# Optimization experiments

Measured on AMD Instinct MI355X. Metric: run time of the kernel, lower is better.

Reference implementation:

```python
import jax, jax.numpy as jnp
import numpy as np
from jax import lax

B, L, D = 2, 1024, 1024
EXPAND, N, K = 2, 16, 4          # expand, d_state, d_conv
DI = EXPAND * D                  # d_inner = 2048
R = (D + 15) // 16               # dt_rank = 64
EPS = 1e-5


def setup_inputs() -> dict:
    key = jax.random.key(0)
    ks = jax.random.split(key, 8)
    x = jax.random.normal(ks[0], (B, L, D), dtype=jnp.float32)
    ln_w = jnp.ones((D,), jnp.float32)
    ln_b = jnp.zeros((D,), jnp.float32)
    W_in = jax.random.normal(ks[1], (D, 2 * DI), jnp.float32) * (1.0 / np.sqrt(D))
    conv_w = jax.random.normal(ks[2], (DI, K), jnp.float32) * 0.2
    conv_b = jnp.zeros((DI,), jnp.float32)
    W_x = jax.random.normal(ks[3], (DI, R + 2 * N), jnp.float32) * (1.0 / np.sqrt(DI))
    W_dt = jax.random.normal(ks[4], (R, DI), jnp.float32) * (1.0 / np.sqrt(R))
    b_dt = jnp.full((DI,), -4.0, jnp.float32)  # softplus(-4) ~ 0.018 dt init
    A_log = jnp.log(jnp.broadcast_to(jnp.arange(1, N + 1, dtype=jnp.float32), (DI, N)))
    D_param = jnp.ones((DI,), jnp.float32)
    W_out = jax.random.normal(ks[5], (DI, D), jnp.float32) * (1.0 / np.sqrt(DI))
    return {"x": x, "ln_w": ln_w, "ln_b": ln_b, "W_in": W_in, "conv_w": conv_w,
            "conv_b": conv_b, "W_x": W_x, "W_dt": W_dt, "b_dt": b_dt,
            "A_log": A_log, "D_param": D_param, "W_out": W_out}


def _mamba_block(x, ln_w, ln_b, W_in, conv_w, conv_b, W_x, W_dt, b_dt, A_log, D_param, W_out):
    # pre-LayerNorm
    mu = jnp.mean(x, axis=-1, keepdims=True)
    xc = x - mu
    var = jnp.mean(xc * xc, axis=-1, keepdims=True)
    h = xc * lax.rsqrt(var + EPS) * ln_w + ln_b          # [B,L,D]

    xz = h @ W_in                                        # [B,L,2*DI]
    xi, z = xz[..., :DI], xz[..., DI:]

    # depthwise causal conv1d, kernel K, left pad K-1
    xp = jnp.pad(xi, ((0, 0), (K - 1, 0), (0, 0)))
    conv = conv_b
    for k in range(K):
        conv = conv + xp[:, k:k + L, :] * conv_w[:, k]
    u = jax.nn.silu(conv)                                # [B,L,DI]

    proj = u @ W_x                                       # [B,L,R+2N]
    dt_r = proj[..., :R]
    Bm = proj[..., R:R + N]                              # [B,L,N]
    Cm = proj[..., R + N:]                               # [B,L,N]
    dt = jax.nn.softplus(dt_r @ W_dt + b_dt)             # [B,L,DI]

    A = -jnp.exp(A_log)                                  # [DI,N]
    dA = jnp.exp(dt[..., None] * A)                      # [B,L,DI,N]
    dBu = (dt * u)[..., None] * Bm[:, :, None, :]        # [B,L,DI,N]

    def comb(e1, e2):
        a1, b1 = e1
        a2, b2 = e2
        return a1 * a2, a2 * b1 + b2

    _, hs = lax.associative_scan(comb, (dA, dBu), axis=1)  # [B,L,DI,N]
    y = jnp.einsum('bldn,bln->bld', hs, Cm) + u * D_param
    y = y * jax.nn.silu(z)
    return x + y @ W_out


def reference(x, ln_w, ln_b, W_in, conv_w, conv_b, W_x, W_dt, b_dt, A_log, D_param, W_out):
    return _mamba_block(x, ln_w, ln_b, W_in, conv_w, conv_b, W_x, W_dt, b_dt,
                        A_log, D_param, W_out)
```

## Files before the change

kernel.cpp:

```cpp
#include <hip/hip_runtime.h>
#include <hip/hip_bf16.h>
#include <math.h>

#define B_ 2
#define L_ 1024
#define D_ 1024
#define DI_ 2048
#define K_ 4
#define N_ 16
#define R_ 64
#define BL_ (B_ * L_)
#define EPS_ 1e-5f

#define IDX4(l) ((l) + (((l) >> 6) << 2))

typedef __attribute__((ext_vector_type(8))) short short8;
typedef __attribute__((ext_vector_type(4))) float f32x4;

__device__ inline unsigned short f2bf(float f) {
    unsigned u = __float_as_uint(f);
    unsigned r = (u + 0x7fffu + ((u >> 16) & 1u)) >> 16;
    return (unsigned short)r;
}
__device__ inline float bf2f(unsigned short s) {
    return __uint_as_float(((unsigned)s) << 16);
}
__device__ inline float fast_silu(float z) {
    return z * __builtin_amdgcn_rcpf(1.f + __expf(-z));
}
__device__ inline void gl_lds16(const void* g, void* l) {
    __builtin_amdgcn_global_load_lds(
        (const __attribute__((address_space(1))) void*)g,
        (__attribute__((address_space(3))) void*)l, 16, 0, 0);
}

template <int CTRL>
__device__ inline float dpp_shr(float x) {
    return __int_as_float(__builtin_amdgcn_update_dpp(
        0, __float_as_int(x), CTRL, 0xf, 0xf, true));
}
__device__ inline float row16_sum(float p) {
    p += dpp_shr<0x111>(p);
    p += dpp_shr<0x112>(p);
    p += dpp_shr<0x114>(p);
    p += dpp_shr<0x118>(p);
    return p;
}

__global__ void ln_kernel(const float* __restrict__ x, const float* __restrict__ w,
                          const float* __restrict__ b, unsigned short* __restrict__ hb) {
    int row = blockIdx.x;
    const float* xr = x + (size_t)row * D_;
    float4 v = ((const float4*)xr)[threadIdx.x];

    __shared__ float red[4];
    float s = v.x + v.y + v.z + v.w;
    for (int off = 1; off < 64; off <<= 1) s += __shfl_xor(s, off, 64);
    if ((threadIdx.x & 63) == 0) red[threadIdx.x >> 6] = s;
    __syncthreads();
    float mu = (red[0] + red[1] + red[2] + red[3]) * (1.0f / D_);
    __syncthreads();
    float cx = v.x - mu, cy = v.y - mu, cz = v.z - mu, cw = v.w - mu;
    float sq = cx*cx + cy*cy + cz*cz + cw*cw;
    for (int off = 1; off < 64; off <<= 1) sq += __shfl_xor(sq, off, 64);
    if ((threadIdx.x & 63) == 0) red[threadIdx.x >> 6] = sq;
    __syncthreads();
    float var = (red[0] + red[1] + red[2] + red[3]) * (1.0f / D_);
    float rstd = rsqrtf(var + EPS_);

    float4 wv = ((const float4*)w)[threadIdx.x];
    float4 bv = ((const float4*)b)[threadIdx.x];
    ushort4 o;
    o.x = f2bf(cx * rstd * wv.x + bv.x);
    o.y = f2bf(cy * rstd * wv.y + bv.y);
    o.z = f2bf(cz * rstd * wv.z + bv.z);
    o.w = f2bf(cw * rstd * wv.w + bv.w);
    ((ushort4*)(hb + (size_t)row * D_))[threadIdx.x] = o;
}

__global__ void transpose_cast_all(const float* __restrict__ W_in, const float* __restrict__ W_x,
                                   const float* __restrict__ W_out,
                                   unsigned short* __restrict__ WinT, unsigned short* __restrict__ WxT,
                                   unsigned short* __restrict__ WoutT) {
    int bid = blockIdx.x;
    const float* W; unsigned short* WT; int K, N, bx, by;
    if (bid < 4096)      { W = W_in;  WT = WinT;  K = 1024; N = 4096; bx = bid & 127; by = bid >> 7; }
    else if (bid < 4288) { int id = bid - 4096; W = W_x;  WT = WxT;  K = DI_; N = 96;   bx = id % 3;  by = id / 3; }
    else                 { int id = bid - 4288; W = W_out; WT = WoutT; K = DI_; N = 1024; bx = id & 31; by = id >> 5; }
    __shared__ float tile[32][33];
    int k0 = by * 32, n0 = bx * 32;
    int tr = threadIdx.x >> 5;
    int tc = threadIdx.x & 31;
#pragma unroll
    for (int i = 0; i < 4; ++i)
        tile[tr + i*8][tc] = W[(size_t)(k0 + tr + i*8) * N + n0 + tc];
    __syncthreads();
#pragma unroll
    for (int i = 0; i < 4; ++i)
        WT[(size_t)(n0 + tr + i*8) * K + k0 + tc] = f2bf(tile[tc][tr + i*8]);
}

template <int BN, int MODE>
__global__ __launch_bounds__(256) void mfma_gemm_bt(
        const unsigned short* __restrict__ A,  int lda,
        const unsigned short* __restrict__ BT, int ldb,
        float* __restrict__ C, int ldc, int Kchunk,
        float* __restrict__ xi, unsigned short* __restrict__ sz) {
    constexpr int NT = BN / 32;
    __shared__ unsigned short As[128 * 32];
    __shared__ unsigned short Bs[BN * 32];

    int tid = threadIdx.x;
    int wave = tid >> 6, lane = tid & 63;
    int lane15 = lane & 15, quad = lane >> 4;
    int wr = wave >> 1, wc = wave & 1;

    int m0 = blockIdx.y * 128;
    int n0 = blockIdx.x * BN;
    int kbeg = blockIdx.z * Kchunk;
    int kend = kbeg + Kchunk;

    f32x4 acc[4][NT];
#pragma unroll
    for (int i = 0; i < 4; ++i)
#pragma unroll
        for (int j = 0; j < NT; ++j) acc[i][j] = (f32x4){0.f, 0.f, 0.f, 0.f};

    constexpr int ACALLS = 8;
    constexpr int BCALLS = BN * 4 / 64;

    for (int k0 = kbeg; k0 < kend; k0 += 32) {
        __syncthreads();
        for (int c = wave; c < ACALLS + BCALLS; c += 4) {
            if (c < ACALLS) {
                int cell = c * 64 + lane;
                int m = cell >> 2, s = cell & 3;
                int q = s ^ (m & 3) ^ ((m >> 2) & 3);
                gl_lds16(A + (size_t)(m0 + m) * lda + k0 + q * 8, &As[c * 512]);
            } else {
                int cell = (c - ACALLS) * 64 + lane;
                int n = cell >> 2, s = cell & 3;
                int q = s ^ (n & 3) ^ ((n >> 2) & 3);
                gl_lds16(BT + (size_t)(n0 + n) * ldb + k0 + q * 8, &Bs[(c - ACALLS) * 512]);
            }
        }
        __syncthreads();

        short8 af[4], bfr[NT];
#pragma unroll
        for (int i = 0; i < 4; ++i) {
            int m = wr * 64 + i * 16 + lane15;
            int s = quad ^ (m & 3) ^ ((m >> 2) & 3);
            af[i] = *(const short8*)&As[m * 32 + s * 8];
        }
#pragma unroll
        for (int j = 0; j < NT; ++j) {
            int n = wc * (NT * 16) + j * 16 + lane15;
            int s = quad ^ (n & 3) ^ ((n >> 2) & 3);
            bfr[j] = *(const short8*)&Bs[n * 32 + s * 8];
        }
#pragma unroll
        for (int i = 0; i < 4; ++i)
#pragma unroll
            for (int j = 0; j < NT; ++j)
                acc[i][j] = __builtin_amdgcn_mfma_f32_16x16x32_bf16(af[i], bfr[j], acc[i][j], 0, 0, 0);
    }

#pragma unroll
    for (int i = 0; i < 4; ++i) {
        int row = m0 + wr * 64 + i * 16 + quad * 4;
#pragma unroll
        for (int j = 0; j < NT; ++j) {
            int col = n0 + wc * (NT * 16) + j * 16 + lane15;
#pragma unroll
            for (int r = 0; r < 4; ++r) {
                float v = acc[i][j][r];
                int rr = row + r;
                if (MODE == 0) {
                    C[(size_t)rr * ldc + col] = v;
                } else if (MODE == 1) {
                    atomicAdd(&C[(size_t)rr * ldc + col], v);
                } else {
                    if (col < DI_) xi[(size_t)rr * DI_ + col] = v;
                    else           sz[(size_t)rr * DI_ + (col - DI_)] = f2bf(fast_silu(v));
                }
            }
        }
    }
}

__global__ void conv_silu_kernel(const float* __restrict__ xi, const float* __restrict__ cw,
                                 const float* __restrict__ cb, unsigned short* __restrict__ ub) {
    int idx = blockIdx.x * blockDim.x + threadIdx.x;
    int c = idx & (DI_ - 1);
    int bl = idx >> 11;
    int l = bl & (L_ - 1);
    float4 w4 = ((const float4*)cw)[c];
    float acc = cb[c];
    const float* base = xi + (size_t)bl * DI_ + c;
    if (l >= 3) {
        acc = fmaf(base[-(size_t)3 * DI_], w4.x, acc);
        acc = fmaf(base[-(size_t)2 * DI_], w4.y, acc);
        acc = fmaf(base[-(size_t)1 * DI_], w4.z, acc);
        acc = fmaf(base[0],                w4.w, acc);
    } else {
        if (l >= 2) acc = fmaf(*(base - 2 * DI_), w4.y, acc);
        if (l >= 1) acc = fmaf(*(base - 1 * DI_), w4.z, acc);
        acc = fmaf(base[0], w4.w, acc);
    }
    ub[idx] = f2bf(fast_silu(acc));
}

__global__ __launch_bounds__(256) void dtprep(
        const float* __restrict__ proj, const float* __restrict__ W_dt,
        const float* __restrict__ b_dt, const unsigned short* __restrict__ ub,
        const unsigned short* __restrict__ szb, const float* __restrict__ Dp,
        float2* __restrict__ dtduT, unsigned int* __restrict__ szdT) {
    __shared__ alignas(16) unsigned char smem[64 * 65 * 8];
    float (*As)[68] = reinterpret_cast<float(*)[68]>(smem);
    float (*Bs)[64] = reinterpret_cast<float(*)[64]>(smem + 4352);
    float2 (*T2)[65] = reinterpret_cast<float2(*)[65]>(smem);
    unsigned int (*TU)[65] = reinterpret_cast<unsigned int(*)[65]>(smem);

    int tid = threadIdx.x;
    int n0 = blockIdx.x * 64;
    int m0 = blockIdx.y * 64;
    int ar = tid >> 2, ak = (tid & 3) << 2;
    int kb = tid >> 4, bc = (tid & 15) << 2;
    int ty = tid >> 4, tx = tid & 15;

    float acc[4][4] = {};
#pragma unroll
    for (int k0 = 0; k0 < R_; k0 += 16) {
        float4 av = *(const float4*)&proj[(size_t)(m0 + ar) * 96 + k0 + ak];
        As[ak + 0][ar] = av.x; As[ak + 1][ar] = av.y;
        As[ak + 2][ar] = av.z; As[ak + 3][ar] = av.w;
        float4 bv = *(const float4*)&W_dt[(size_t)(k0 + kb) * DI_ + n0 + bc];
        Bs[kb][bc + 0] = bv.x; Bs[kb][bc + 1] = bv.y;
        Bs[kb][bc + 2] = bv.z; Bs[kb][bc + 3] = bv.w;
        __syncthreads();
#pragma unroll
        for (int kk = 0; kk < 16; ++kk) {
            float a[4], bb[4];
#pragma unroll
            for (int i = 0; i < 4; ++i) a[i] = As[kk][ty * 4 + i];
#pragma unroll
            for (int j = 0; j < 4; ++j) bb[j] = Bs[kk][tx * 4 + j];
#pragma unroll
            for (int i = 0; i < 4; ++i)
#pragma unroll
                for (int j = 0; j < 4; ++j)
                    acc[i][j] = fmaf(a[i], bb[j], acc[i][j]);
        }
        __syncthreads();
    }

    float4 bd = *(const float4*)&b_dt[n0 + tx * 4];
    float4 dp4 = *(const float4*)&Dp[n0 + tx * 4];
    float bda[4] = {bd.x, bd.y, bd.z, bd.w};
    float dpa[4] = {dp4.x, dp4.y, dp4.z, dp4.w};
    float2 d2[4][4];
    unsigned int su[4][4];
#pragma unroll
    for (int i = 0; i < 4; ++i) {
        int bl = m0 + ty * 4 + i;
        ushort4 u4 = *(const ushort4*)&ub[(size_t)bl * DI_ + n0 + tx * 4];
        ushort4 s4 = *(const ushort4*)&szb[(size_t)bl * DI_ + n0 + tx * 4];
        unsigned short ua[4] = {u4.x, u4.y, u4.z, u4.w};
        unsigned short sa[4] = {s4.x, s4.y, s4.z, s4.w};
#pragma unroll
        for (int j = 0; j < 4; ++j) {
            float v = acc[i][j] + bda[j];
            float dtv = fmaxf(v, 0.f) + __logf(1.f + __expf(-fabsf(v)));
            float uu = bf2f(ua[j]);
            float szv = bf2f(sa[j]);
            d2[i][j] = make_float2(dtv, dtv * uu);
            su[i][j] = ((unsigned)f2bf(uu * dpa[j] * szv) << 16) | (unsigned)f2bf(szv);
        }
    }

#pragma unroll
    for (int i = 0; i < 4; ++i)
#pragma unroll
        for (int j = 0; j < 4; ++j)
            T2[ty * 4 + i][tx * 4 + j] = d2[i][j];
    __syncthreads();
#pragma unroll
    for (int i = 0; i < 8; ++i) {
        int c_l = (tid >> 5) + i * 8;
#pragma unroll
        for (int jj = 0; jj < 2; ++jj) {
            int bl_l = (tid & 31) + jj * 32;
            dtduT[(size_t)(n0 + c_l) * BL_ + m0 + bl_l] = T2[bl_l][c_l];
        }
    }
    __syncthreads();

#pragma unroll
    for (int i = 0; i < 4; ++i)
#pragma unroll
        for (int j = 0; j < 4; ++j)
            TU[ty * 4 + i][tx * 4 + j] = su[i][j];
    __syncthreads();
#pragma unroll
    for (int i = 0; i < 8; ++i) {
        int c_l = (tid >> 5) + i * 8;
#pragma unroll
        for (int jj = 0; jj < 2; ++jj) {
            int bl_l = (tid & 31) + jj * 32;
            szdT[(size_t)(n0 + c_l) * BL_ + m0 + bl_l] = TU[bl_l][c_l];
        }
    }
}

__global__ __launch_bounds__(256) void scan_v5(
        const float2* __restrict__ dtduT, const unsigned int* __restrict__ szdT,
        const float* __restrict__ proj, const float* __restrict__ A_log,
        unsigned short* __restrict__ yzT) {
    int bc = blockIdx.x;
    int b = bc >> 10;
    int cp = bc & 1023;
    int t = threadIdx.x;
    int n = t & 15;
    int cs = (t >> 4) & 1;
    int chunk = t >> 5;
    int c = cp * 2 + cs;

    __shared__ float dd[2][(L_ + 32) * 2];
    __shared__ float sA[8][32];
    __shared__ float sB[8][32];
    __shared__ float ps[2][L_ + 64];

    {
        int half = t >> 7;
        int tt = t & 127;
        int l = tt * 8;
        int cload = cp * 2 + half;
        const float4* g = (const float4*)(dtduT + (size_t)cload * BL_ + (size_t)b * L_ + l);
        int il2 = l + ((l >> 6) << 1);
        float* dst = &dd[half][il2 * 2];
        *(float4*)(dst + 0)  = g[0];
        *(float4*)(dst + 4)  = g[1];
        *(float4*)(dst + 8)  = g[2];
        *(float4*)(dst + 12) = g[3];
    }
    __syncthreads();

    float A = -__expf(A_log[c * N_ + n]);
    int l0 = chunk * 128;
    const float* pB = proj + (size_t)b * L_ * 96 + R_ + n;
    const float* pC = pB + N_;

    float a = 1.f, acc = 0.f;
#pragma unroll
    for (int h = 0; h < 2; ++h) {
        int lb = l0 + h * 64;
        const float* ddp = &dd[cs][(lb + ((lb >> 6) << 1)) * 2];
        const float* pBb = pB + (size_t)lb * 96;
#pragma unroll
        for (int q = 0; q < 16; ++q) {
            float4 d0 = *(const float4*)(ddp + q * 8);
            float4 d1 = *(const float4*)(ddp + q * 8 + 4);
            float b0 = pBb[(q*4 + 0) * 96];
            float b1 = pBb[(q*4 + 1) * 96];
            float b2 = pBb[(q*4 + 2) * 96];
            float b3 = pBb[(q*4 + 3) * 96];
            float e;
            e = __expf(d0.x * A); a *= e; acc = fmaf(e, acc, d0.y * b0);
            e = __expf(d0.z * A); a *= e; acc = fmaf(e, acc, d0.w * b1);
            e = __expf(d1.x * A); a *= e; acc = fmaf(e, acc, d1.y * b2);
            e = __expf(d1.z * A); a *= e; acc = fmaf(e, acc, d1.w * b3);
        }
    }
    sA[chunk][t & 31] = a;
    sB[chunk][t & 31] = acc;
    __syncthreads();

    if (t < 32) {
        float hc = 0.f;
#pragma unroll
        for (int j = 0; j < 8; ++j) {
            float aj = sA[j][t];
            float bj = sB[j][t];
            sB[j][t] = hc;
            hc = fmaf(aj, hc, bj);
        }
    }
    __syncthreads();
    float h = sB[chunk][t & 31];

#pragma unroll
    for (int hh = 0; hh < 2; ++hh) {
        int lb = l0 + hh * 64;
        const float* ddp = &dd[cs][(lb + ((lb >> 6) << 1)) * 2];
        const float* pBb = pB + (size_t)lb * 96;
        const float* pCb = pC + (size_t)lb * 96;
        float* psb = &ps[cs][IDX4(lb)];
#pragma unroll
        for (int q = 0; q < 16; ++q) {
            float4 d0 = *(const float4*)(ddp + q * 8);
            float4 d1 = *(const float4*)(ddp + q * 8 + 4);
            float b0 = pBb[(q*4 + 0) * 96], c0 = pCb[(q*4 + 0) * 96];
            float b1 = pBb[(q*4 + 1) * 96], c1 = pCb[(q*4 + 1) * 96];
            float b2 = pBb[(q*4 + 2) * 96], c2 = pCb[(q*4 + 2) * 96];
            float b3 = pBb[(q*4 + 3) * 96], c3 = pCb[(q*4 + 3) * 96];
            float e, p0, p1, p2, p3;
            e = __expf(d0.x * A); h = fmaf(e, h, d0.y * b0); p0 = row16_sum(h * c0);
            e = __expf(d0.z * A); h = fmaf(e, h, d0.w * b1); p1 = row16_sum(h * c1);
            e = __expf(d1.x * A); h = fmaf(e, h, d1.y * b2); p2 = row16_sum(h * c2);
            e = __expf(d1.z * A); h = fmaf(e, h, d1.w * b3); p3 = row16_sum(h * c3);
            if (n == 15) *(float4*)&psb[q * 4] = (float4){p0, p1, p2, p3};
        }
    }
    __syncthreads();

    {
        int half = t >> 7;
        int tt = t & 127;
        int l = tt * 8;
        int c_out = cp * 2 + half;
        size_t tb = (size_t)c_out * BL_ + (size_t)b * L_;
        const float* pp = &ps[half][IDX4(l)];
        ushort4 o[2];
#pragma unroll
        for (int g = 0; g < 2; ++g) {
            float4 p4 = *(const float4*)(pp + g * 4);
            uint4 sd4 = *(const uint4*)(szdT + tb + l + g * 4);
            o[g].x = f2bf(p4.x * bf2f((unsigned short)(sd4.x & 0xffff)) + bf2f((unsigned short)(sd4.x >> 16)));
            o[g].y = f2bf(p4.y * bf2f((unsigned short)(sd4.y & 0xffff)) + bf2f((unsigned short)(sd4.y >> 16)));
            o[g].z = f2bf(p4.z * bf2f((unsigned short)(sd4.z & 0xffff)) + bf2f((unsigned short)(sd4.z >> 16)));
            o[g].w = f2bf(p4.w * bf2f((unsigned short)(sd4.w & 0xffff)) + bf2f((unsigned short)(sd4.w >> 16)));
        }
        *(ushort4*)(yzT + tb + l) = o[0];
        *(ushort4*)(yzT + tb + l + 4) = o[1];
    }
}

__global__ void transpose_y(const unsigned short* __restrict__ yzT, unsigned short* __restrict__ yz) {
    __shared__ unsigned short t[32][33];
    int c0 = blockIdx.y * 32, bl0 = blockIdx.x * 32;
    int r = threadIdx.x >> 5;
    int col = threadIdx.x & 31;
#pragma unroll
    for (int i = 0; i < 4; ++i)
        t[r + i*8][col] = yzT[(size_t)(c0 + r + i*8) * BL_ + bl0 + col];
    __syncthreads();
#pragma unroll
    for (int i = 0; i < 4; ++i)
        yz[(size_t)(bl0 + r + i*8) * DI_ + c0 + col] = t[col][r + i*8];
}

extern "C" void kernel_launch(void* const* d_in, const int* in_sizes, int n_in,
                              void* d_out, int out_size, void* d_ws, size_t ws_size,
                              hipStream_t stream) {
    const float* x       = (const float*)d_in[0];
    const float* ln_w    = (const float*)d_in[1];
    const float* ln_b    = (const float*)d_in[2];
    const float* W_in    = (const float*)d_in[3];
    const float* conv_w  = (const float*)d_in[4];
    const float* conv_b  = (const float*)d_in[5];
    const float* W_x     = (const float*)d_in[6];
    const float* W_dt    = (const float*)d_in[7];
    const float* b_dt    = (const float*)d_in[8];
    const float* A_log   = (const float*)d_in[9];
    const float* D_param = (const float*)d_in[10];
    const float* W_out   = (const float*)d_in[11];
    float* out = (float*)d_out;

    uint8_t* p = (uint8_t*)d_ws;
    unsigned short* hb    = (unsigned short*)p;  p += (size_t)BL_ * D_ * 2;
    unsigned short* WinT  = (unsigned short*)p;  p += (size_t)4096 * 1024 * 2;
    float*          xib   = (float*)p;           p += (size_t)BL_ * DI_ * 4;
    unsigned short* szb   = (unsigned short*)p;  p += (size_t)BL_ * DI_ * 2;
    unsigned short* ub    = (unsigned short*)p;  p += (size_t)BL_ * DI_ * 2;
    unsigned short* WxT   = (unsigned short*)p;  p += (size_t)96 * DI_ * 2;
    float*          proj  = (float*)p;           p += (size_t)BL_ * 96 * 4;
    unsigned short* WoutT = (unsigned short*)p;  p += (size_t)1024 * DI_ * 2;
    float2*         dtduT = (float2*)p;          p += (size_t)BL_ * DI_ * 8;
    unsigned int*   szdT  = (unsigned int*)p;    p += (size_t)BL_ * DI_ * 4;
    unsigned short* yzT   = (unsigned short*)p;  p += (size_t)BL_ * DI_ * 2;
    unsigned short* yzb   = (unsigned short*)d_ws;

    hipMemsetAsync(proj, 0, (size_t)BL_ * 96 * 4, stream);
    hipMemcpyAsync(out, x, (size_t)BL_ * D_ * 4, hipMemcpyDeviceToDevice, stream);

    transpose_cast_all<<<6336, 256, 0, stream>>>(W_in, W_x, W_out, WinT, WxT, WoutT);

    ln_kernel<<<BL_, 256, 0, stream>>>(x, ln_w, ln_b, hb);

    mfma_gemm_bt<128, 3><<<dim3(4096 / 128, BL_ / 128, 1), 256, 0, stream>>>(
        hb, 1024, WinT, 1024, nullptr, 0, 1024, xib, szb);

    conv_silu_kernel<<<(BL_ * DI_) / 256, 256, 0, stream>>>(xib, conv_w, conv_b, ub);

    mfma_gemm_bt<96, 1><<<dim3(1, BL_ / 128, 16), 256, 0, stream>>>(
        ub, DI_, WxT, DI_, proj, 96, 128, nullptr, nullptr);

    dtprep<<<dim3(DI_ / 64, BL_ / 64), 256, 0, stream>>>(
        proj, W_dt, b_dt, ub, szb, D_param, dtduT, szdT);

    scan_v5<<<B_ * DI_ / 2, 256, 0, stream>>>(dtduT, szdT, proj, A_log, yzT);

    transpose_y<<<dim3(BL_ / 32, DI_ / 32), 256, 0, stream>>>(yzT, yzb);

    mfma_gemm_bt<128, 1><<<dim3(1024 / 128, BL_ / 128, 2), 256, 0, stream>>>(
        yzb, DI_, WoutT, DI_, out, 1024, 1024, nullptr, nullptr);
}
```

Before: 285.6 us.

## Transpose B/C to contiguous layout and run scan with one channel per block

A new small kernel transposes the B and C columns of proj into [b][n][l] arrays, so each scan thread reads them as contiguous float4 instead of scalar loads strided by 96. The scan now gives each block a single channel with 16 chunks of 64 steps, which doubles the block count, shortens each thread's sequential work, and adds a launch-bounds occupancy hint. The exponentials become hardware exp2 with log2(e) folded into A. In exchange there is one extra kernel launch, a longer 16-step chunk-carry pass, and BT/CT are placed in a workspace region assumed not to overlap live buffers.

```diff
diff --git a/kernel.cpp b/kernel.cpp
--- a/kernel.cpp
+++ b/kernel.cpp
@@ -28,6 +28,11 @@
 __device__ inline float fast_silu(float z) {
     return z * __builtin_amdgcn_rcpf(1.f + __expf(-z));
 }
+#if __has_builtin(__builtin_amdgcn_exp2f)
+__device__ inline float fexp2(float x) { return __builtin_amdgcn_exp2f(x); }
+#else
+__device__ inline float fexp2(float x) { return exp2f(x); }
+#endif
 __device__ inline void gl_lds16(const void* g, void* l) {
     __builtin_amdgcn_global_load_lds(
         (const __attribute__((address_space(1))) void*)g,
@@ -313,73 +318,79 @@
     }
 }
 
-__global__ __launch_bounds__(256) void scan_v5(
+__global__ void bc_transpose(const float* __restrict__ proj,
+                             float* __restrict__ BT, float* __restrict__ CT) {
+    __shared__ float t[32][33];
+    int bl0 = blockIdx.x * 32;
+    int b = bl0 >> 10;
+    int l0 = bl0 & (L_ - 1);
+    int r = threadIdx.x >> 5;
+    int col = threadIdx.x & 31;
+#pragma unroll
+    for (int i = 0; i < 4; ++i)
+        t[r + i*8][col] = proj[(size_t)(bl0 + r + i*8) * 96 + R_ + col];
+    __syncthreads();
+#pragma unroll
+    for (int i = 0; i < 4; ++i) {
+        int n = r + i*8;
+        float v = t[col][n];
+        if (n < N_) BT[((size_t)b * N_ + n) * L_ + l0 + col] = v;
+        else        CT[((size_t)b * N_ + (n - N_)) * L_ + l0 + col] = v;
+    }
+}
+
+__global__ __launch_bounds__(256, 6) void scan_v6(
         const float2* __restrict__ dtduT, const unsigned int* __restrict__ szdT,
-        const float* __restrict__ proj, const float* __restrict__ A_log,
-        unsigned short* __restrict__ yzT) {
+        const float* __restrict__ BT, const float* __restrict__ CT,
+        const float* __restrict__ A_log, unsigned short* __restrict__ yzT) {
     int bc = blockIdx.x;
-    int b = bc >> 10;
-    int cp = bc & 1023;
+    int b = bc >> 11;
+    int c = bc & (DI_ - 1);
     int t = threadIdx.x;
     int n = t & 15;
-    int cs = (t >> 4) & 1;
-    int chunk = t >> 5;
-    int c = cp * 2 + cs;
-
-    __shared__ float dd[2][(L_ + 32) * 2];
-    __shared__ float sA[8][32];
-    __shared__ float sB[8][32];
-    __shared__ float ps[2][L_ + 64];
+    int chunk = t >> 4;
+
+    __shared__ float dd[(L_ + 32) * 2];
+    __shared__ float sA[16][16];
+    __shared__ float sB[16][16];
+    __shared__ float ps[L_ + 64];
 
     {
-        int half = t >> 7;
-        int tt = t & 127;
-        int l = tt * 8;
-        int cload = cp * 2 + half;
-        const float4* g = (const float4*)(dtduT + (size_t)cload * BL_ + (size_t)b * L_ + l);
+        int l = t * 4;
+        const float4* g = (const float4*)(dtduT + (size_t)c * BL_ + (size_t)b * L_ + l);
         int il2 = l + ((l >> 6) << 1);
-        float* dst = &dd[half][il2 * 2];
-        *(float4*)(dst + 0)  = g[0];
-        *(float4*)(dst + 4)  = g[1];
-        *(float4*)(dst + 8)  = g[2];
-        *(float4*)(dst + 12) = g[3];
-    }
-    __syncthreads();
-
-    float A = -__expf(A_log[c * N_ + n]);
-    int l0 = chunk * 128;
-    const float* pB = proj + (size_t)b * L_ * 96 + R_ + n;
-    const float* pC = pB + N_;
+        float* dst = &dd[il2 * 2];
+        *(float4*)(dst + 0) = g[0];
+        *(float4*)(dst + 4) = g[1];
+    }
+    __syncthreads();
+
+    float A2 = -__expf(A_log[c * N_ + n]) * 1.4426950408889634f;
+    int lb = chunk * 64;
+    const float* ddp = &dd[(lb + ((lb >> 6) << 1)) * 2];
+    const float4* pB4 = (const float4*)(BT + ((size_t)b * N_ + n) * L_ + lb);
+    const float4* pC4 = (const float4*)(CT + ((size_t)b * N_ + n) * L_ + lb);
 
     float a = 1.f, acc = 0.f;
 #pragma unroll
-    for (int h = 0; h < 2; ++h) {
-        int lb = l0 + h * 64;
-        const float* ddp = &dd[cs][(lb + ((lb >> 6) << 1)) * 2];
-        const float* pBb = pB + (size_t)lb * 96;
-#pragma unroll
-        for (int q = 0; q < 16; ++q) {
-            float4 d0 = *(const float4*)(ddp + q * 8);
-            float4 d1 = *(const float4*)(ddp + q * 8 + 4);
-            float b0 = pBb[(q*4 + 0) * 96];
-            float b1 = pBb[(q*4 + 1) * 96];
-            float b2 = pBb[(q*4 + 2) * 96];
-            float b3 = pBb[(q*4 + 3) * 96];
-            float e;
-            e = __expf(d0.x * A); a *= e; acc = fmaf(e, acc, d0.y * b0);
-            e = __expf(d0.z * A); a *= e; acc = fmaf(e, acc, d0.w * b1);
-            e = __expf(d1.x * A); a *= e; acc = fmaf(e, acc, d1.y * b2);
-            e = __expf(d1.z * A); a *= e; acc = fmaf(e, acc, d1.w * b3);
-        }
-    }
-    sA[chunk][t & 31] = a;
-    sB[chunk][t & 31] = acc;
-    __syncthreads();
-
-    if (t < 32) {
+    for (int q = 0; q < 16; ++q) {
+        float4 d0 = *(const float4*)(ddp + q * 8);
+        float4 d1 = *(const float4*)(ddp + q * 8 + 4);
+        float4 b4 = pB4[q];
+        float e;
+        e = fexp2(d0.x * A2); a *= e; acc = fmaf(e, acc, d0.y * b4.x);
+        e = fexp2(d0.z * A2); a *= e; acc = fmaf(e, acc, d0.w * b4.y);
+        e = fexp2(d1.x * A2); a *= e; acc = fmaf(e, acc, d1.y * b4.z);
+        e = fexp2(d1.z * A2); a *= e; acc = fmaf(e, acc, d1.w * b4.w);
+    }
+    sA[chunk][n] = a;
+    sB[chunk][n] = acc;
+    __syncthreads();
+
+    if (t < 16) {
         float hc = 0.f;
 #pragma unroll
-        for (int j = 0; j < 8; ++j) {
+        for (int j = 0; j < 16; ++j) {
             float aj = sA[j][t];
             float bj = sB[j][t];
             sB[j][t] = hc;
@@ -387,52 +398,36 @@
         }
     }
     __syncthreads();
-    float h = sB[chunk][t & 31];
-
-#pragma unroll
-    for (int hh = 0; hh < 2; ++hh) {
-        int lb = l0 + hh * 64;
-        const float* ddp = &dd[cs][(lb + ((lb >> 6) << 1)) * 2];
-        const float* pBb = pB + (size_t)lb * 96;
-        const float* pCb = pC + (size_t)lb * 96;
-        float* psb = &ps[cs][IDX4(lb)];
-#pragma unroll
-        for (int q = 0; q < 16; ++q) {
-            float4 d0 = *(const float4*)(ddp + q * 8);
-            float4 d1 = *(const float4*)(ddp + q * 8 + 4);
-            float b0 = pBb[(q*4 + 0) * 96], c0 = pCb[(q*4 + 0) * 96];
-            float b1 = pBb[(q*4 + 1) * 96], c1 = pCb[(q*4 + 1) * 96];
-            float b2 = pBb[(q*4 + 2) * 96], c2 = pCb[(q*4 + 2) * 96];
-            float b3 = pBb[(q*4 + 3) * 96], c3 = pCb[(q*4 + 3) * 96];
-            float e, p0, p1, p2, p3;
-            e = __expf(d0.x * A); h = fmaf(e, h, d0.y * b0); p0 = row16_sum(h * c0);
-            e = __expf(d0.z * A); h = fmaf(e, h, d0.w * b1); p1 = row16_sum(h * c1);
-            e = __expf(d1.x * A); h = fmaf(e, h, d1.y * b2); p2 = row16_sum(h * c2);
-            e = __expf(d1.z * A); h = fmaf(e, h, d1.w * b3); p3 = row16_sum(h * c3);
-            if (n == 15) *(float4*)&psb[q * 4] = (float4){p0, p1, p2, p3};
-        }
+    float h = sB[chunk][n];
+
+    float* psb = &ps[IDX4(lb)];
+#pragma unroll
+    for (int q = 0; q < 16; ++q) {
+        float4 d0 = *(const float4*)(ddp + q * 8);
+        float4 d1 = *(const float4*)(ddp + q * 8 + 4);
+        float4 b4 = pB4[q];
+        float4 c4 = pC4[q];
+        float e, p0, p1, p2, p3;
+        e = fexp2(d0.x * A2); h = fmaf(e, h, d0.y * b4.x); p0 = row16_sum(h * c4.x);
+        e = fexp2(d0.z * A2); h = fmaf(e, h, d0.w * b4.y); p1 = row16_sum(h * c4.y);
+        e = fexp2(d1.x * A2); h = fmaf(e, h, d1.y * b4.z); p2 = row16_sum(h * c4.z);
+        e = fexp2(d1.z * A2); h = fmaf(e, h, d1.w * b4.w); p3 = row16_sum(h * c4.w);
+        if (n == 15) *(float4*)&psb[q * 4] = (float4){p0, p1, p2, p3};
     }
     __syncthreads();
 
     {
-        int half = t >> 7;
-        int tt = t & 127;
-        int l = tt * 8;
-        int c_out = cp * 2 + half;
-        size_t tb = (size_t)c_out * BL_ + (size_t)b * L_;
-        const float* pp = &ps[half][IDX4(l)];
-        ushort4 o[2];
-#pragma unroll
-        for (int g = 0; g < 2; ++g) {
-            float4 p4 = *(const float4*)(pp + g * 4);
-            uint4 sd4 = *(const uint4*)(szdT + tb + l + g * 4);
-            o[g].x = f2bf(p4.x * bf2f((unsigned short)(sd4.x & 0xffff)) + bf2f((unsigned short)(sd4.x >> 16)));
-            o[g].y = f2bf(p4.y * bf2f((unsigned short)(sd4.y & 0xffff)) + bf2f((unsigned short)(sd4.y >> 16)));
-            o[g].z = f2bf(p4.z * bf2f((unsigned short)(sd4.z & 0xffff)) + bf2f((unsigned short)(sd4.z >> 16)));
-            o[g].w = f2bf(p4.w * bf2f((unsigned short)(sd4.w & 0xffff)) + bf2f((unsigned short)(sd4.w >> 16)));
-        }
-        *(ushort4*)(yzT + tb + l) = o[0];
-        *(ushort4*)(yzT + tb + l + 4) = o[1];
+        int l = t * 4;
+        size_t tb = (size_t)c * BL_ + (size_t)b * L_;
+        const float* pp = &ps[IDX4(l)];
+        float4 p4 = *(const float4*)pp;
+        uint4 sd4 = *(const uint4*)(szdT + tb + l);
+        ushort4 o;
+        o.x = f2bf(p4.x * bf2f((unsigned short)(sd4.x & 0xffff)) + bf2f((unsigned short)(sd4.x >> 16)));
+        o.y = f2bf(p4.y * bf2f((unsigned short)(sd4.y & 0xffff)) + bf2f((unsigned short)(sd4.y >> 16)));
+        o.z = f2bf(p4.z * bf2f((unsigned short)(sd4.z & 0xffff)) + bf2f((unsigned short)(sd4.z >> 16)));
+        o.w = f2bf(p4.w * bf2f((unsigned short)(sd4.w & 0xffff)) + bf2f((unsigned short)(sd4.w >> 16)));
+        *(ushort4*)(yzT + tb + l) = o;
     }
 }
 
@@ -480,6 +475,8 @@
     unsigned int*   szdT  = (unsigned int*)p;    p += (size_t)BL_ * DI_ * 4;
     unsigned short* yzT   = (unsigned short*)p;  p += (size_t)BL_ * DI_ * 2;
     unsigned short* yzb   = (unsigned short*)d_ws;
+    float*          BT    = (float*)((uint8_t*)d_ws + (size_t)8 * 1024 * 1024);
+    float*          CT    = BT + (size_t)B_ * N_ * L_;
 
     hipMemsetAsync(proj, 0, (size_t)BL_ * 96 * 4, stream);
     hipMemcpyAsync(out, x, (size_t)BL_ * D_ * 4, hipMemcpyDeviceToDevice, stream);
@@ -496,10 +493,12 @@
     mfma_gemm_bt<96, 1><<<dim3(1, BL_ / 128, 16), 256, 0, stream>>>(
         ub, DI_, WxT, DI_, proj, 96, 128, nullptr, nullptr);
 
+    bc_transpose<<<BL_ / 32, 256, 0, stream>>>(proj, BT, CT);
+
     dtprep<<<dim3(DI_ / 64, BL_ / 64), 256, 0, stream>>>(
         proj, W_dt, b_dt, ub, szb, D_param, dtduT, szdT);
 
-    scan_v5<<<B_ * DI_ / 2, 256, 0, stream>>>(dtduT, szdT, proj, A_log, yzT);
+    scan_v6<<<B_ * DI_, 256, 0, stream>>>(dtduT, szdT, BT, CT, A_log, yzT);
 
     transpose_y<<<dim3(BL_ / 32, DI_ / 32), 256, 0, stream>>>(yzT, yzb);
 
```

New measurement: 396.0 us. 38.6% more time.
